# Performance work log

Hardware: AMD Instinct MI355X
Metric: run time of the kernel (lower is better)

## Reference

```python
import jax, jax.numpy as jnp
import numpy as np

B, T = 64, 2048
D, H, L, OUT, V = 128, 256, 2, 64, 1000


def lstm_layer(x, Wih, Whh, bih, bhh):
    """Single-direction LSTM layer, PyTorch gate order (i, f, g, o).
    x: [B, T, Din] -> [B, T, H]"""
    Bn = x.shape[0]
    Hh = Whh.shape[1]
    # precompute input contribution to gates once: [B, T, 4H] -> time-major
    xg = jnp.einsum('btd,gd->btg', x, Wih) + bih
    xg = jnp.swapaxes(xg, 0, 1)  # [T, B, 4H]

    def step(carry, g_x):
        h, c = carry
        g = g_x + h @ Whh.T + bhh
        i, f, gg, o = jnp.split(g, 4, axis=-1)
        c = jax.nn.sigmoid(f) * c + jax.nn.sigmoid(i) * jnp.tanh(gg)
        h = jax.nn.sigmoid(o) * jnp.tanh(c)
        return (h, c), h

    h0 = jnp.zeros((Bn, Hh), x.dtype)
    (_, _), hs = jax.lax.scan(step, (h0, h0), xg)
    return jnp.swapaxes(hs, 0, 1)  # [B, T, H]


def setup_inputs() -> dict:
    key = jax.random.key(0)
    ks = jax.random.split(key, 12)
    s = 0.05
    inp = {
        'x': jax.random.randint(ks[0], (B, T), 0, V + 1, dtype=jnp.int32),
        'embed_table': jax.random.normal(ks[1], (V + 1, D), jnp.float32) * s,
        'W_ih0': jax.random.normal(ks[2], (4 * H, D), jnp.float32) * s,
        'W_hh0': jax.random.normal(ks[3], (4 * H, H), jnp.float32) * s,
        'b_ih0': jax.random.normal(ks[4], (4 * H,), jnp.float32) * s,
        'b_hh0': jax.random.normal(ks[5], (4 * H,), jnp.float32) * s,
        'W_ih1': jax.random.normal(ks[6], (4 * H, H), jnp.float32) * s,
        'W_hh1': jax.random.normal(ks[7], (4 * H, H), jnp.float32) * s,
        'b_ih1': jax.random.normal(ks[8], (4 * H,), jnp.float32) * s,
        'b_hh1': jax.random.normal(ks[9], (4 * H,), jnp.float32) * s,
        'fc_W': jax.random.normal(ks[10], (OUT, H), jnp.float32) * s,
        'fc_b': jax.random.normal(ks[11], (OUT,), jnp.float32) * s,
    }
    return inp


def reference(x, embed_table, W_ih0, W_hh0, b_ih0, b_hh0,
              W_ih1, W_hh1, b_ih1, b_hh1, fc_W, fc_b):
    # embedding + padding mask (padding_idx=0, masked_fill x==0 -> 0)
    e = embed_table[x]                              # [B, T, D]
    e = e * (x != 0)[..., None].astype(e.dtype)
    # 2-layer LSTM, zero initial state
    h = lstm_layer(e, W_ih0, W_hh0, b_ih0, b_hh0)   # [B, T, H]
    h = lstm_layer(h, W_ih1, W_hh1, b_ih1, b_hh1)   # [B, T, H]
    # linear + softmax over last dim
    logits = jnp.einsum('bth,oh->bto', h, fc_W) + fc_b
    return jax.nn.softmax(logits, axis=-1)
```

## Files before the change

### kernel.cpp

```cpp
#include <hip/hip_runtime.h>
#include <cstdint>
#include <cstddef>


typedef _Float16 half_t;
typedef _Float16 half8 __attribute__((ext_vector_type(8)));
typedef _Float16 half2t __attribute__((ext_vector_type(2)));
typedef float floatx4 __attribute__((ext_vector_type(4)));

#define B_   64
#define T_   2048
#define D_   128
#define H_   256
#define G4_  1024
#define OUT_ 64
#define MTOT (B_ * T_)

#define RF4 48
#define LF4 16
#define LDS4_BYTES (8 * LF4 * 64 * 16)

#if defined(__has_builtin)
#if __has_builtin(__builtin_amdgcn_fdot2)
#define HAVE_FDOT2 1
#endif
#endif

__device__ __forceinline__ float dot2acc(unsigned w, unsigned h, float acc) {
  half2t a = __builtin_bit_cast(half2t, w);
  half2t b = __builtin_bit_cast(half2t, h);
#ifdef HAVE_FDOT2
  return __builtin_amdgcn_fdot2(a, b, acc, false);
#else
  return acc + (float)a[0] * (float)b[0] + (float)a[1] * (float)b[1];
#endif
}

__device__ __forceinline__ float fast_sigmoid(float x) {
  return 1.f / (1.f + __expf(-x));
}
__device__ __forceinline__ float fast_tanh(float x) {
  return 1.f - 2.f / (1.f + __expf(2.f * x));
}


__global__ __launch_bounds__(256) void k_cvt_f16(const float* __restrict__ in,
                                                 half_t* __restrict__ out, int n) {
  int i = blockIdx.x * 256 + threadIdx.x;
  if (i < n) out[i] = (half_t)in[i];
}

__global__ __launch_bounds__(256) void k_pack_whh(const float* __restrict__ whh,
                                                  half_t* __restrict__ wp) {
  int i = blockIdx.x * 256 + threadIdx.x;
  int e  = i & 7;
  int j  = (i >> 3) & 1023;
  int kc = i >> 13;
  wp[i] = (half_t)whh[j * 256 + kc * 8 + e];
}

__global__ __launch_bounds__(256) void k_pack_whh_frag(const float* __restrict__ whh,
                                                       half_t* __restrict__ wqf) {
  int i = blockIdx.x * 256 + threadIdx.x;
  int e  = i & 7;
  int l  = (i >> 3) & 63;
  int kc = (i >> 9) & 7;
  int rt = (i >> 12) & 15;
  int w  = (i >> 16) & 3;
  int row = w * 256 + rt * 16 + (l & 15);
  int col = kc * 32 + (l >> 4) * 8 + e;
  wqf[i] = (half_t)whh[row * 256 + col];
}

__global__ __launch_bounds__(256) void k_bias(const float* __restrict__ a,
                                              const float* __restrict__ b,
                                              float* __restrict__ out, int n) {
  int i = blockIdx.x * 256 + threadIdx.x;
  if (i < n) out[i] = a[i] + b[i];
}

__global__ __launch_bounds__(256) void k_fcwt(const float* __restrict__ fcw,
                                              float* __restrict__ fcwt) {
  int i = blockIdx.x * 256 + threadIdx.x;
  fcwt[i] = fcw[(i & 63) * 256 + (i >> 6)];
}


__global__ __launch_bounds__(256) void k_embed(const int* __restrict__ x,
                                               const float* __restrict__ tab,
                                               half_t* __restrict__ e) {
  const long i = (long)blockIdx.x * 256 + threadIdx.x;
  const long m = i >> 4;
  const int ch = (int)(i & 15) * 8;
  const int xi = x[m];
  half8 v;
  #pragma unroll
  for (int q = 0; q < 8; ++q) v[q] = (half_t)0.f;
  if (xi != 0) {
    const float* p = tab + (long)xi * D_ + ch;
    #pragma unroll
    for (int q = 0; q < 8; ++q) v[q] = (half_t)p[q];
  }
  *(half8*)(e + m * D_ + ch) = v;
}


__global__ __launch_bounds__(256) void k_gemm_f16(const half_t* __restrict__ A,
                                                  const half_t* __restrict__ Wt,
                                                  const float* __restrict__ bias,
                                                  half_t* __restrict__ C,
                                                  int K, int N,
                                                  int rowShift, int strideB, int toff) {
  __shared__ half_t As[128][40];
  __shared__ half_t Bs[128][40];
  const int tid  = threadIdx.x;
  const int lane = tid & 63;
  const int wave = tid >> 6;
  const int wr = wave >> 1, wc = wave & 1;
  const int r0 = blockIdx.x * 128;
  const int n0 = blockIdx.y * 128;
  const int srow = tid >> 2;
  const int schunk = (tid & 3) * 8;
  const int rmask = (1 << rowShift) - 1;

  floatx4 zero = {0.f, 0.f, 0.f, 0.f};
  floatx4 acc[4][4];
  for (int i = 0; i < 4; ++i)
    for (int j = 0; j < 4; ++j) acc[i][j] = zero;

  const int ra = r0 + srow, rb = r0 + srow + 64;
  const half_t* ArowA = A + ((long)(ra >> rowShift) * strideB + toff + (ra & rmask)) * K;
  const half_t* ArowB = A + ((long)(rb >> rowShift) * strideB + toff + (rb & rmask)) * K;

  for (int k0 = 0; k0 < K; k0 += 32) {
    *(uint4*)(&As[srow][schunk])      = *(const uint4*)(ArowA + k0 + schunk);
    *(uint4*)(&As[srow + 64][schunk]) = *(const uint4*)(ArowB + k0 + schunk);
    const half_t* Bp = Wt + (long)(n0 + srow) * K + k0 + schunk;
    *(uint4*)(&Bs[srow][schunk])      = *(const uint4*)(Bp);
    *(uint4*)(&Bs[srow + 64][schunk]) = *(const uint4*)(Bp + 64L * K);
    __syncthreads();

    const int kq = (lane >> 4) * 8;
    const int fr = lane & 15;
    half8 af[4], bf[4];
    #pragma unroll
    for (int i = 0; i < 4; ++i) af[i] = *(const half8*)(&As[wr * 64 + i * 16 + fr][kq]);
    #pragma unroll
    for (int i = 0; i < 4; ++i) bf[i] = *(const half8*)(&Bs[wc * 64 + i * 16 + fr][kq]);
    #pragma unroll
    for (int mi = 0; mi < 4; ++mi)
      #pragma unroll
      for (int ni = 0; ni < 4; ++ni)
        acc[mi][ni] = __builtin_amdgcn_mfma_f32_16x16x32_f16(af[mi], bf[ni], acc[mi][ni], 0, 0, 0);
    __syncthreads();
  }

  const int fr = lane & 15, fq = lane >> 4;
  for (int ni = 0; ni < 4; ++ni) {
    const int gcol = n0 + wc * 64 + ni * 16 + fr;
    const float bv = bias[gcol];
    for (int mi = 0; mi < 4; ++mi) {
      const long grow = r0 + wr * 64 + mi * 16 + fq * 4;
      #pragma unroll
      for (int r = 0; r < 4; ++r)
        C[(grow + r) * (long)N + gcol] = (half_t)(acc[mi][ni][r] + bv);
    }
  }
}


__global__ __launch_bounds__(512, 2) void k_lstm_v4(const half_t* __restrict__ xg,
                                                    const uint4* __restrict__ wqf,
                                                    half_t* __restrict__ hout,
                                                    float* __restrict__ c_state,
                                                    half_t* __restrict__ h_state,
                                                    int steps, int first) {
  extern __shared__ uint4 wlds[];
  __shared__ __align__(16) half_t hsh[2][256];
  __shared__ __align__(16) float gsh[1024];
  const int b = blockIdx.x;
  const int tid = threadIdx.x;
  const int w = tid >> 6, l = tid & 63;
  const int q = l >> 4;

  const uint4* wbase = wqf + ((size_t)(w >> 1) * 128 + (size_t)(w & 1) * 64) * 64;
  half8 wv[RF4];
  #pragma unroll
  for (int i = 0; i < RF4; ++i)
    wv[i] = __builtin_bit_cast(half8, wbase[i * 64 + l]);
  #pragma unroll
  for (int i = 0; i < LF4; ++i)
    wlds[(w * LF4 + i) * 64 + l] = wbase[(RF4 + i) * 64 + l];

  float c = 0.f;
  float xc0 = 0.f, xc1 = 0.f, xc2 = 0.f, xc3 = 0.f;
  const half_t* xgb = xg + (long)b * steps * G4_;
  if (tid < 256) {
    if (first) {
      hsh[0][tid] = (half_t)0.f;
    } else {
      hsh[0][tid] = h_state[b * H_ + tid];
      c = c_state[b * H_ + tid];
    }
    xc0 = (float)xgb[tid];
    xc1 = (float)xgb[256 + tid];
    xc2 = (float)xgb[512 + tid];
    xc3 = (float)xgb[768 + tid];
  }
  __syncthreads();

  half_t* hp_out = hout + (long)b * steps * H_ + tid;

  for (int t = 0; t < steps; ++t) {
    float xn0 = 0.f, xn1 = 0.f, xn2 = 0.f, xn3 = 0.f;
    if (tid < 256) {
      const half_t* xrn = xgb + (long)((t + 1 < steps) ? t + 1 : t) * G4_;
      xn0 = (float)xrn[tid];
      xn1 = (float)xrn[256 + tid];
      xn2 = (float)xrn[512 + tid];
      xn3 = (float)xrn[768 + tid];
    }

    const half_t* hp = hsh[t & 1];
    floatx4 acc[4];

    #pragma unroll
    for (int i = 0; i < 4; ++i) acc[i] = (floatx4){0.f, 0.f, 0.f, 0.f};
    #pragma unroll
    for (int kb = 0; kb < 2; ++kb) {
      half8 bf4[4];
      #pragma unroll
      for (int kk = 0; kk < 4; ++kk)
        bf4[kk] = *(const half8*)(hp + (kb * 4 + kk) * 32 + (q << 3));
      #pragma unroll
      for (int kk = 0; kk < 4; ++kk)
        #pragma unroll
        for (int rt = 0; rt < 4; ++rt)
          acc[rt] = __builtin_amdgcn_mfma_f32_16x16x32_f16(
              wv[rt * 8 + kb * 4 + kk], bf4[kk], acc[rt], 0, 0, 0);
    }
    if ((l & 15) == 0) {
      #pragma unroll
      for (int rt = 0; rt < 4; ++rt)
        *(floatx4*)&gsh[w * 128 + rt * 16 + (q << 2)] = acc[rt];
    }

    #pragma unroll
    for (int i = 0; i < 4; ++i) acc[i] = (floatx4){0.f, 0.f, 0.f, 0.f};
    #pragma unroll
    for (int kb = 0; kb < 2; ++kb) {
      half8 bf4[4];
      #pragma unroll
      for (int kk = 0; kk < 4; ++kk)
        bf4[kk] = *(const half8*)(hp + (kb * 4 + kk) * 32 + (q << 3));
      #pragma unroll
      for (int kk = 0; kk < 4; ++kk) {
        const int kc = kb * 4 + kk;
        #pragma unroll
        for (int rt = 0; rt < 2; ++rt)
          acc[rt] = __builtin_amdgcn_mfma_f32_16x16x32_f16(
              wv[(4 + rt) * 8 + kc], bf4[kk], acc[rt], 0, 0, 0);
        #pragma unroll
        for (int rt = 0; rt < 2; ++rt) {
          half8 wf = __builtin_bit_cast(half8,
              wlds[(w * LF4 + rt * 8 + kc) * 64 + l]);
          acc[2 + rt] = __builtin_amdgcn_mfma_f32_16x16x32_f16(
              wf, bf4[kk], acc[2 + rt], 0, 0, 0);
        }
      }
    }
    if ((l & 15) == 0) {
      #pragma unroll
      for (int rt = 0; rt < 4; ++rt)
        *(floatx4*)&gsh[w * 128 + (4 + rt) * 16 + (q << 2)] = acc[rt];
    }
    __syncthreads();

    if (tid < 256) {
      float gi = gsh[tid]       + xc0;
      float gf = gsh[256 + tid] + xc1;
      float gg = gsh[512 + tid] + xc2;
      float go = gsh[768 + tid] + xc3;
      float ig = fast_sigmoid(gi);
      float fg = fast_sigmoid(gf);
      float g2 = fast_tanh(gg);
      float og = fast_sigmoid(go);
      c = fg * c + ig * g2;
      float h = og * fast_tanh(c);
      half_t hh = (half_t)h;
      hp_out[(long)t * H_] = hh;
      hsh[(t + 1) & 1][tid] = hh;
    }
    xc0 = xn0; xc1 = xn1; xc2 = xn2; xc3 = xn3;
    __syncthreads();
  }
  if (tid < 256) {
    c_state[b * H_ + tid] = c;
    h_state[b * H_ + tid] = hsh[steps & 1][tid];
  }
}


__global__ __launch_bounds__(1024) void k_lstm(const half_t* __restrict__ xg,
                                               const uint4* __restrict__ Wp,
                                               half_t* __restrict__ hout,
                                               float* __restrict__ c_state,
                                               half_t* __restrict__ h_state,
                                               int steps, int first) {
  const int b = blockIdx.x;
  const int j = threadIdx.x;
  __shared__ float gsh[1024];
  __shared__ __align__(16) half_t hsh[256];
  float c = 0.f;
  if (j < H_) {
    if (first) {
      hsh[j] = (half_t)0.f;
    } else {
      hsh[j] = h_state[b * H_ + j];
      c = c_state[b * H_ + j];
    }
  }
  const uint4*  wp     = Wp + j;
  const half_t* xp     = xg + (long)b * steps * G4_ + j;
  half_t*       hp_out = hout + (long)b * steps * H_;
  for (int t = 0; t < steps; ++t) {
    __syncthreads();
    float acc = (float)xp[(long)t * G4_];
    const uint4* hv4 = (const uint4*)hsh;
    #pragma unroll 8
    for (int kc = 0; kc < 32; ++kc) {
      uint4 w  = wp[(long)kc * G4_];
      uint4 h4 = hv4[kc];
      acc = dot2acc(w.x, h4.x, acc);
      acc = dot2acc(w.y, h4.y, acc);
      acc = dot2acc(w.z, h4.z, acc);
      acc = dot2acc(w.w, h4.w, acc);
    }
    gsh[j] = acc;
    __syncthreads();
    if (j < H_) {
      float ig = fast_sigmoid(gsh[j]);
      float fg = fast_sigmoid(gsh[H_ + j]);
      float g2 = fast_tanh(gsh[2 * H_ + j]);
      float og = fast_sigmoid(gsh[3 * H_ + j]);
      c = fg * c + ig * g2;
      float h = og * fast_tanh(c);
      hp_out[(long)t * H_ + j] = (half_t)h;
      hsh[j] = (half_t)h;
    }
  }
  if (j < H_) {
    c_state[b * H_ + j] = c;
    h_state[b * H_ + j] = hsh[j];
  }
}


__global__ __launch_bounds__(256) void k_fc_softmax(const half_t* __restrict__ h2,
                                                    const float* __restrict__ fcwt,
                                                    const float* __restrict__ fcb,
                                                    float* __restrict__ out,
                                                    int rowShift, int strideB, int toff) {
  const int lane = threadIdx.x & 63;
  const int r = blockIdx.x * 4 + (threadIdx.x >> 6);
  const half_t* hr = h2 + (long)r * H_;
  float acc = fcb[lane];
  for (int kc = 0; kc < 32; ++kc) {
    uint4 hv = *(const uint4*)(hr + kc * 8);
    unsigned hu[4] = {hv.x, hv.y, hv.z, hv.w};
    #pragma unroll
    for (int p = 0; p < 4; ++p) {
      half2t hh = __builtin_bit_cast(half2t, hu[p]);
      acc += (float)hh[0] * fcwt[(kc * 8 + p * 2) * 64 + lane];
      acc += (float)hh[1] * fcwt[(kc * 8 + p * 2 + 1) * 64 + lane];
    }
  }
  float m = acc;
  #pragma unroll
  for (int off = 32; off > 0; off >>= 1) m = fmaxf(m, __shfl_xor(m, off));
  float e = __expf(acc - m);
  float s = e;
  #pragma unroll
  for (int off = 32; off > 0; off >>= 1) s += __shfl_xor(s, off);
  const long outrow = (long)(r >> rowShift) * strideB + toff + (r & ((1 << rowShift) - 1));
  out[outrow * OUT_ + lane] = e / s;
}


extern "C" void kernel_launch(void* const* d_in, const int* in_sizes, int n_in,
                              void* d_out, int out_size, void* d_ws, size_t ws_size,
                              hipStream_t stream) {
  const int*   x    = (const int*)d_in[0];
  const float* tab  = (const float*)d_in[1];
  const float* wih0 = (const float*)d_in[2];
  const float* whh0 = (const float*)d_in[3];
  const float* bih0 = (const float*)d_in[4];
  const float* bhh0 = (const float*)d_in[5];
  const float* wih1 = (const float*)d_in[6];
  const float* whh1 = (const float*)d_in[7];
  const float* bih1 = (const float*)d_in[8];
  const float* bhh1 = (const float*)d_in[9];
  const float* fcw  = (const float*)d_in[10];
  const float* fcb  = (const float*)d_in[11];

  char* p = (char*)d_ws;
  auto alloc = [&](size_t bytes) {
    void* r = (void*)p;
    p += (bytes + 255) & ~(size_t)255;
    return r;
  };
  half_t* wih0_h = (half_t*)alloc((size_t)G4_ * D_ * 2);
  half_t* wih1_h = (half_t*)alloc((size_t)G4_ * H_ * 2);
  half_t* wqf0   = (half_t*)alloc((size_t)G4_ * H_ * 2);
  half_t* wqf1   = (half_t*)alloc((size_t)G4_ * H_ * 2);
  half_t* wp0    = (half_t*)alloc((size_t)G4_ * H_ * 2);
  half_t* wp1    = (half_t*)alloc((size_t)G4_ * H_ * 2);
  float*  bias0  = (float*)alloc(G4_ * 4);
  float*  bias1  = (float*)alloc(G4_ * 4);
  float*  fcwt   = (float*)alloc((size_t)H_ * OUT_ * 4);
  half_t* hstate = (half_t*)alloc((size_t)2 * B_ * H_ * 2);
  float*  cstate = (float*)alloc((size_t)2 * B_ * H_ * 4);
  size_t fixed_used = (size_t)(p - (char*)d_ws);

  int CH = 2048;
  while (CH > 32 &&
         fixed_used + (size_t)CH * (131072 + 32768) + (1u << 20) > ws_size)
    CH >>= 1;
  const int rowShift = __builtin_ctz(CH);
  half_t* XG = (half_t*)alloc((size_t)CH * B_ * G4_ * 2);
  half_t* HB = (half_t*)alloc((size_t)CH * B_ * H_ * 2);
  half_t* ebuf = (half_t*)d_out;

  hipError_t attr_rc = hipFuncSetAttribute(
      reinterpret_cast<const void*>(k_lstm_v4),
      hipFuncAttributeMaxDynamicSharedMemorySize, LDS4_BYTES);
  const bool use_res = (attr_rc == hipSuccess);

  k_cvt_f16<<<512, 256, 0, stream>>>(wih0, wih0_h, G4_ * D_);
  k_cvt_f16<<<1024, 256, 0, stream>>>(wih1, wih1_h, G4_ * H_);
  k_pack_whh_frag<<<1024, 256, 0, stream>>>(whh0, wqf0);
  k_pack_whh_frag<<<1024, 256, 0, stream>>>(whh1, wqf1);
  k_pack_whh<<<1024, 256, 0, stream>>>(whh0, wp0);
  k_pack_whh<<<1024, 256, 0, stream>>>(whh1, wp1);
  k_bias<<<4, 256, 0, stream>>>(bih0, bhh0, bias0, G4_);
  k_bias<<<4, 256, 0, stream>>>(bih1, bhh1, bias1, G4_);
  k_fcwt<<<64, 256, 0, stream>>>(fcw, fcwt);

  k_embed<<<MTOT * (D_ / 8) / 256, 256, 0, stream>>>(x, tab, ebuf);

  const int M = B_ * CH;
  const int nchunks = T_ / CH;
  for (int ci = 0; ci < nchunks; ++ci) {
    const int t0 = ci * CH;
    k_gemm_f16<<<dim3(M / 128, G4_ / 128), 256, 0, stream>>>(
        ebuf, wih0_h, bias0, XG, D_, G4_, rowShift, T_, t0);
    if (use_res)
      k_lstm_v4<<<B_, 512, LDS4_BYTES, stream>>>(XG, (const uint4*)wqf0, HB,
                                                 cstate, hstate, CH, ci == 0);
    else
      k_lstm<<<B_, 1024, 0, stream>>>(XG, (const uint4*)wp0, HB,
                                      cstate, hstate, CH, ci == 0);
    k_gemm_f16<<<dim3(M / 128, G4_ / 128), 256, 0, stream>>>(
        HB, wih1_h, bias1, XG, H_, G4_, rowShift, CH, 0);
    if (use_res)
      k_lstm_v4<<<B_, 512, LDS4_BYTES, stream>>>(XG, (const uint4*)wqf1, HB,
                                                 cstate + B_ * H_, hstate + B_ * H_,
                                                 CH, ci == 0);
    else
      k_lstm<<<B_, 1024, 0, stream>>>(XG, (const uint4*)wp1, HB,
                                      cstate + B_ * H_, hstate + B_ * H_,
                                      CH, ci == 0);
    k_fc_softmax<<<M / 4, 256, 0, stream>>>(HB, fcwt, fcb, (float*)d_out,
                                            rowShift, T_, t0);
  }
}
```

Before: 7.985 ms.

## Interleave gate rows so each wave applies the LSTM cell in registers

The recurrent weight fragments are repacked so the four gates of a hidden unit share one MFMA output tile. Each wave can then apply sigmoid/tanh and update the cell state directly from its accumulators, which removes the gate round trip through shared memory and one of the two barriers per timestep. The next step's input projection is now staged through a double-buffered LDS array. In exchange, only one lane in 16 does the activation math, so that work becomes serialized within each wave.

```diff
diff --git a/kernel.cpp b/kernel.cpp
--- a/kernel.cpp
+++ b/kernel.cpp
@@ -16,9 +16,9 @@
 #define OUT_ 64
 #define MTOT (B_ * T_)
 
-#define RF4 48
-#define LF4 16
-#define LDS4_BYTES (8 * LF4 * 64 * 16)
+#define RF5 48
+#define LF5 16
+#define LDS5_BYTES (8 * LF5 * 64 * 16)
 
 #if defined(__has_builtin)
 #if __has_builtin(__builtin_amdgcn_fdot2)
@@ -59,17 +59,19 @@
   wp[i] = (half_t)whh[j * 256 + kc * 8 + e];
 }
 
-__global__ __launch_bounds__(256) void k_pack_whh_frag(const float* __restrict__ whh,
-                                                       half_t* __restrict__ wqf) {
+__global__ __launch_bounds__(256) void k_pack_whh_frag2(const float* __restrict__ whh,
+                                                        half_t* __restrict__ wqf2) {
   int i = blockIdx.x * 256 + threadIdx.x;
   int e  = i & 7;
   int l  = (i >> 3) & 63;
   int kc = (i >> 9) & 7;
-  int rt = (i >> 12) & 15;
-  int w  = (i >> 16) & 3;
-  int row = w * 256 + rt * 16 + (l & 15);
+  int rt = (i >> 12) & 7;
+  int w  = (i >> 15) & 7;
+  int ri = l & 15;
+  int g  = ri & 3;
+  int u  = w * 32 + rt * 4 + (ri >> 2);
   int col = kc * 32 + (l >> 4) * 8 + e;
-  wqf[i] = (half_t)whh[row * 256 + col];
+  wqf2[i] = (half_t)whh[(g * 256 + u) * 256 + col];
 }
 
 __global__ __launch_bounds__(256) void k_bias(const float* __restrict__ a,
@@ -169,59 +171,55 @@
 }
 
 
-__global__ __launch_bounds__(512, 2) void k_lstm_v4(const half_t* __restrict__ xg,
-                                                    const uint4* __restrict__ wqf,
+__global__ __launch_bounds__(512, 2) void k_lstm_v5(const half_t* __restrict__ xg,
+                                                    const uint4* __restrict__ wqf2,
                                                     half_t* __restrict__ hout,
                                                     float* __restrict__ c_state,
                                                     half_t* __restrict__ h_state,
                                                     int steps, int first) {
   extern __shared__ uint4 wlds[];
   __shared__ __align__(16) half_t hsh[2][256];
-  __shared__ __align__(16) float gsh[1024];
+  __shared__ __align__(16) half_t xlds[2][1024];
   const int b = blockIdx.x;
   const int tid = threadIdx.x;
   const int w = tid >> 6, l = tid & 63;
   const int q = l >> 4;
-
-  const uint4* wbase = wqf + ((size_t)(w >> 1) * 128 + (size_t)(w & 1) * 64) * 64;
-  half8 wv[RF4];
-  #pragma unroll
-  for (int i = 0; i < RF4; ++i)
+  const bool owner = ((l & 15) == 0);
+
+  const uint4* wbase = wqf2 + (size_t)w * 64 * 64;
+  half8 wv[RF5];
+  #pragma unroll
+  for (int i = 0; i < RF5; ++i)
     wv[i] = __builtin_bit_cast(half8, wbase[i * 64 + l]);
   #pragma unroll
-  for (int i = 0; i < LF4; ++i)
-    wlds[(w * LF4 + i) * 64 + l] = wbase[(RF4 + i) * 64 + l];
-
-  float c = 0.f;
-  float xc0 = 0.f, xc1 = 0.f, xc2 = 0.f, xc3 = 0.f;
+  for (int i = 0; i < LF5; ++i)
+    wlds[(w * LF5 + i) * 64 + l] = wbase[(RF5 + i) * 64 + l];
+
   const half_t* xgb = xg + (long)b * steps * G4_;
-  if (tid < 256) {
-    if (first) {
-      hsh[0][tid] = (half_t)0.f;
-    } else {
-      hsh[0][tid] = h_state[b * H_ + tid];
-      c = c_state[b * H_ + tid];
-    }
-    xc0 = (float)xgb[tid];
-    xc1 = (float)xgb[256 + tid];
-    xc2 = (float)xgb[512 + tid];
-    xc3 = (float)xgb[768 + tid];
+  half_t* hob = hout + (long)b * steps * H_;
+
+  float creg[8];
+  #pragma unroll
+  for (int rt = 0; rt < 8; ++rt) creg[rt] = 0.f;
+  if (tid < 256)
+    hsh[0][tid] = first ? (half_t)0.f : h_state[b * H_ + tid];
+  if (owner && !first) {
+    #pragma unroll
+    for (int rt = 0; rt < 8; ++rt)
+      creg[rt] = c_state[b * H_ + w * 32 + rt * 4 + q];
+  }
+  {
+    unsigned v = *(const unsigned*)(xgb + tid * 2);
+    *(unsigned*)&xlds[0][tid * 2] = v;
   }
   __syncthreads();
 
-  half_t* hp_out = hout + (long)b * steps * H_ + tid;
-
   for (int t = 0; t < steps; ++t) {
-    float xn0 = 0.f, xn1 = 0.f, xn2 = 0.f, xn3 = 0.f;
-    if (tid < 256) {
-      const half_t* xrn = xgb + (long)((t + 1 < steps) ? t + 1 : t) * G4_;
-      xn0 = (float)xrn[tid];
-      xn1 = (float)xrn[256 + tid];
-      xn2 = (float)xrn[512 + tid];
-      xn3 = (float)xrn[768 + tid];
-    }
+    const int tn = (t + 1 < steps) ? t + 1 : t;
+    unsigned xv = *(const unsigned*)(xgb + (long)tn * G4_ + tid * 2);
 
     const half_t* hp = hsh[t & 1];
+    const half_t* xp = xlds[t & 1];
     floatx4 acc[4];
 
     #pragma unroll
@@ -239,10 +237,20 @@
           acc[rt] = __builtin_amdgcn_mfma_f32_16x16x32_f16(
               wv[rt * 8 + kb * 4 + kk], bf4[kk], acc[rt], 0, 0, 0);
     }
-    if ((l & 15) == 0) {
-      #pragma unroll
-      for (int rt = 0; rt < 4; ++rt)
-        *(floatx4*)&gsh[w * 128 + rt * 16 + (q << 2)] = acc[rt];
+    if (owner) {
+      #pragma unroll
+      for (int rt = 0; rt < 4; ++rt) {
+        const int u = w * 32 + rt * 4 + q;
+        float ig = fast_sigmoid(acc[rt][0] + (float)xp[u]);
+        float fg = fast_sigmoid(acc[rt][1] + (float)xp[256 + u]);
+        float g2 = fast_tanh(acc[rt][2] + (float)xp[512 + u]);
+        float og = fast_sigmoid(acc[rt][3] + (float)xp[768 + u]);
+        creg[rt] = fg * creg[rt] + ig * g2;
+        float h = og * fast_tanh(creg[rt]);
+        half_t hh = (half_t)h;
+        hsh[(t + 1) & 1][u] = hh;
+        hob[(long)t * H_ + u] = hh;
+      }
     }
 
     #pragma unroll
@@ -263,40 +271,38 @@
         #pragma unroll
         for (int rt = 0; rt < 2; ++rt) {
           half8 wf = __builtin_bit_cast(half8,
-              wlds[(w * LF4 + rt * 8 + kc) * 64 + l]);
+              wlds[(w * LF5 + rt * 8 + kc) * 64 + l]);
           acc[2 + rt] = __builtin_amdgcn_mfma_f32_16x16x32_f16(
               wf, bf4[kk], acc[2 + rt], 0, 0, 0);
         }
       }
     }
-    if ((l & 15) == 0) {
-      #pragma unroll
-      for (int rt = 0; rt < 4; ++rt)
-        *(floatx4*)&gsh[w * 128 + (4 + rt) * 16 + (q << 2)] = acc[rt];
-    }
+    if (owner) {
+      #pragma unroll
+      for (int rt = 0; rt < 4; ++rt) {
+        const int u = w * 32 + (4 + rt) * 4 + q;
+        float ig = fast_sigmoid(acc[rt][0] + (float)xp[u]);
+        float fg = fast_sigmoid(acc[rt][1] + (float)xp[256 + u]);
+        float g2 = fast_tanh(acc[rt][2] + (float)xp[512 + u]);
+        float og = fast_sigmoid(acc[rt][3] + (float)xp[768 + u]);
+        creg[4 + rt] = fg * creg[4 + rt] + ig * g2;
+        float h = og * fast_tanh(creg[4 + rt]);
+        half_t hh = (half_t)h;
+        hsh[(t + 1) & 1][u] = hh;
+        hob[(long)t * H_ + u] = hh;
+      }
+    }
+
+    *(unsigned*)&xlds[(t + 1) & 1][tid * 2] = xv;
     __syncthreads();
-
-    if (tid < 256) {
-      float gi = gsh[tid]       + xc0;
-      float gf = gsh[256 + tid] + xc1;
-      float gg = gsh[512 + tid] + xc2;
-      float go = gsh[768 + tid] + xc3;
-      float ig = fast_sigmoid(gi);
-      float fg = fast_sigmoid(gf);
-      float g2 = fast_tanh(gg);
-      float og = fast_sigmoid(go);
-      c = fg * c + ig * g2;
-      float h = og * fast_tanh(c);
-      half_t hh = (half_t)h;
-      hp_out[(long)t * H_] = hh;
-      hsh[(t + 1) & 1][tid] = hh;
-    }
-    xc0 = xn0; xc1 = xn1; xc2 = xn2; xc3 = xn3;
-    __syncthreads();
-  }
-  if (tid < 256) {
-    c_state[b * H_ + tid] = c;
+  }
+
+  if (tid < 256)
     h_state[b * H_ + tid] = hsh[steps & 1][tid];
+  if (owner) {
+    #pragma unroll
+    for (int rt = 0; rt < 8; ++rt)
+      c_state[b * H_ + w * 32 + rt * 4 + q] = creg[rt];
   }
 }
 
@@ -432,14 +438,14 @@
   half_t* ebuf = (half_t*)d_out;
 
   hipError_t attr_rc = hipFuncSetAttribute(
-      reinterpret_cast<const void*>(k_lstm_v4),
-      hipFuncAttributeMaxDynamicSharedMemorySize, LDS4_BYTES);
+      reinterpret_cast<const void*>(k_lstm_v5),
+      hipFuncAttributeMaxDynamicSharedMemorySize, LDS5_BYTES);
   const bool use_res = (attr_rc == hipSuccess);
 
   k_cvt_f16<<<512, 256, 0, stream>>>(wih0, wih0_h, G4_ * D_);
   k_cvt_f16<<<1024, 256, 0, stream>>>(wih1, wih1_h, G4_ * H_);
-  k_pack_whh_frag<<<1024, 256, 0, stream>>>(whh0, wqf0);
-  k_pack_whh_frag<<<1024, 256, 0, stream>>>(whh1, wqf1);
+  k_pack_whh_frag2<<<1024, 256, 0, stream>>>(whh0, wqf0);
+  k_pack_whh_frag2<<<1024, 256, 0, stream>>>(whh1, wqf1);
   k_pack_whh<<<1024, 256, 0, stream>>>(whh0, wp0);
   k_pack_whh<<<1024, 256, 0, stream>>>(whh1, wp1);
   k_bias<<<4, 256, 0, stream>>>(bih0, bhh0, bias0, G4_);
@@ -455,7 +461,7 @@
     k_gemm_f16<<<dim3(M / 128, G4_ / 128), 256, 0, stream>>>(
         ebuf, wih0_h, bias0, XG, D_, G4_, rowShift, T_, t0);
     if (use_res)
-      k_lstm_v4<<<B_, 512, LDS4_BYTES, stream>>>(XG, (const uint4*)wqf0, HB,
+      k_lstm_v5<<<B_, 512, LDS5_BYTES, stream>>>(XG, (const uint4*)wqf0, HB,
                                                  cstate, hstate, CH, ci == 0);
     else
       k_lstm<<<B_, 1024, 0, stream>>>(XG, (const uint4*)wp0, HB,
@@ -463,7 +469,7 @@
     k_gemm_f16<<<dim3(M / 128, G4_ / 128), 256, 0, stream>>>(
         HB, wih1_h, bias1, XG, H_, G4_, rowShift, CH, 0);
     if (use_res)
-      k_lstm_v4<<<B_, 512, LDS4_BYTES, stream>>>(XG, (const uint4*)wqf1, HB,
+      k_lstm_v5<<<B_, 512, LDS5_BYTES, stream>>>(XG, (const uint4*)wqf1, HB,
                                                  cstate + B_ * H_, hstate + B_ * H_,
                                                  CH, ci == 0);
     else
```

Result: slower. 21.61 ms (+170.6%).
